# Kernel tuning notes

Hardware: AMD Instinct MI355X
Metric: run time of the kernel (lower is better)

Reference implementation:

```python
import jax, jax.numpy as jnp
import numpy as np


def _chain_marginals(u, p, g):
    """Gamma-smoothed forward-backward marginals on independent chains.
    u: [N, L, K] unaries, p: [N, L-1, K, K] pairwise (prev-state, next-state), g: scalar temperature.
    Returns marginals [N, L, K] (softmax of smoothed max-marginals).
    """
    u_t = jnp.swapaxes(u, 0, 1)   # [L, N, K]
    p_t = jnp.swapaxes(p, 0, 1)   # [L-1, N, K, K]

    def fstep(a, xs):
        ui, pi = xs  # ui: [N,K] at i, pi: [N,K,K] edge (i-1,i)
        a_new = ui + g * jax.nn.logsumexp((a[:, :, None] + pi) / g, axis=1)
        return a_new, a_new

    a0 = u_t[0]
    _, alpha_rest = jax.lax.scan(fstep, a0, (u_t[1:], p_t))
    alpha = jnp.concatenate([a0[None], alpha_rest], axis=0)  # [L,N,K]

    def bstep(b, xs):
        ui, pi = xs  # ui: unary at i+1, pi: edge (i, i+1)
        b_new = g * jax.nn.logsumexp(((ui + b)[:, None, :] + pi) / g, axis=2)
        return b_new, b_new

    bL = jnp.zeros_like(a0)
    _, beta_head = jax.lax.scan(bstep, bL, (u_t[1:], p_t), reverse=True)
    beta = jnp.concatenate([beta_head, bL[None]], axis=0)  # [L,N,K]

    m = jax.nn.softmax((alpha + beta) / g, axis=-1)
    return jnp.swapaxes(m, 0, 1)  # [N,L,K]


def setup_inputs() -> dict:
    key = jax.random.key(0)
    ks = jax.random.split(key, 4)
    B, K, H, W = 4, 21, 256, 256
    return {
        "unary_h": jax.random.normal(ks[0], (B, K, H, W), dtype=jnp.float32),
        "unary_v": jax.random.normal(ks[1], (B, K, H, W), dtype=jnp.float32),
        "pairwise_h": jax.random.normal(ks[2], (B, K, K, H, W - 1), dtype=jnp.float32),
        "pairwise_v": jax.random.normal(ks[3], (B, K, K, H - 1, W), dtype=jnp.float32),
        "gamma": jnp.ones((1,), dtype=jnp.float32),
    }


def reference(unary_h, unary_v, pairwise_h, pairwise_v, gamma):
    g = jnp.maximum(gamma[0], 0.01)  # module clamps learned gamma to >= 0.01
    B, K, H, W = unary_h.shape

    # Horizontal chains: one chain per (b, h) row, length W.
    uh = unary_h.transpose(0, 2, 3, 1).reshape(B * H, W, K)
    ph = pairwise_h.transpose(0, 3, 4, 1, 2).reshape(B * H, W - 1, K, K)
    mh = _chain_marginals(uh, ph, g).reshape(B, H, W, K).transpose(0, 3, 1, 2)

    # Vertical chains: one chain per (b, w) column, length H.
    uv = unary_v.transpose(0, 3, 2, 1).reshape(B * W, H, K)
    pv = pairwise_v.transpose(0, 4, 3, 1, 2).reshape(B * W, H - 1, K, K)
    mv = _chain_marginals(uv, pv, g).reshape(B, W, H, K).transpose(0, 3, 2, 1)

    avg = (mh + mv) * 0.5
    new_uh = unary_h - (mh - avg) / W
    new_uv = unary_v - (mv - avg) / H
    return new_uh, new_uv, mh, mv
```

## Files before the change

### kernel.cpp

```cpp
#include <hip/hip_runtime.h>


#define K 21
#define KP 22
#define TT 8
#define HP 256
#define NE 255
#define ROWF (K*KP)
#define TILEF (TT*ROWF)
#define EUF (TT*K)
#define NT 32
#define SZ (4*K*HP*HP)

__device__ __forceinline__ float rlane(float v, int l) {
  return __int_as_float(__builtin_amdgcn_readlane(__float_as_int(v), l));
}

__global__ __launch_bounds__(384)
void fp_scan_kernel(const float* __restrict__ uh, const float* __restrict__ uv,
                    const float* __restrict__ ph, const float* __restrict__ pv,
                    const float* __restrict__ gam, float* out) {
  __shared__ float smem[2*TILEF + 2*EUF];
  const float g = fmaxf(gam[0], 0.01f);
  const float invg = 1.0f / g;
  float* outMH = out + 2L*SZ;
  float* outMV = out + 3L*SZ;
  const int wg = blockIdx.x;
  const int tid = threadIdx.x;

  if (wg < 64) {
    const int b   = wg >> 4;
    const int wc0 = (wg & 15) << 4;
    const int kIdx = tid >> 4;
    const int c    = tid & 15;
    const int kk   = (kIdx < K) ? kIdx : (K-1);
    const bool pred = (kIdx < K);
    float* bc = smem;

    const long uBase = ((long)(b*K + kk)*HP)*HP + wc0 + c;
    const long kStep = (long)NE*HP;

    float pA[K], pB[K];

    {
      const long pfBase = (((long)(b*K)*K + kk)*NE)*HP + wc0 + c;
      float ea = __expf(uv[uBase] * invg);
      if (pred) outMV[uBase] = ea;
      #pragma unroll
      for (int k2 = 0; k2 < K; ++k2) pA[k2] = pv[pfBase + (long)k2*K*kStep];
      float uA = uv[uBase + 1L*HP], uB;

      auto fstep = [&](int i, const float* P, float uN, float ea_) -> float {
        bc[(i&1)*336 + kk*16 + c] = ea_;
        __syncthreads();
        const float* bb = bc + (i&1)*336 + c;
        float y0 = fmaxf(bb[0], 1e-33f);
        float s0=0.f, s1=0.f, s2=0.f;
        #pragma unroll
        for (int k2 = 0; k2 < K; k2 += 3) {
          s0 = fmaf(__expf(P[k2  ]*invg), bb[(k2  )*16], s0);
          s1 = fmaf(__expf(P[k2+1]*invg), bb[(k2+1)*16], s1);
          s2 = fmaf(__expf(P[k2+2]*invg), bb[(k2+2)*16], s2);
        }
        float r = (((s0+s1)+s2) / y0) * __expf(uN*invg);
        if (pred) outMV[uBase + (long)(i+1)*HP] = r;
        return r;
      };

      for (int i = 0; i < 254; i += 2) {
        #pragma unroll
        for (int k2=0;k2<K;++k2) pB[k2] = pv[pfBase + (long)k2*K*kStep + (long)(i+1)*HP];
        uB = uv[uBase + (long)(i+2)*HP];
        ea = fstep(i, pA, uA, ea);
        #pragma unroll
        for (int k2=0;k2<K;++k2) pA[k2] = pv[pfBase + (long)k2*K*kStep + (long)(i+2)*HP];
        uA = uv[uBase + (long)(i+3)*HP];
        ea = fstep(i+1, pB, uB, ea);
      }
      ea = fstep(254, pA, uA, ea);
    }
    __syncthreads();
    {
      const long pbBase = (((long)(b*K + kk)*K)*NE)*HP + wc0 + c;
      float eb = 1.0f;
      #pragma unroll
      for (int k2=0;k2<K;++k2) pA[k2] = pv[pbBase + (long)k2*kStep + 254L*HP];
      float uA  = uv[uBase + 255L*HP], uB;
      float eaA = outMV[uBase + 254L*HP], eaB;

      auto bstep = [&](int i, const float* P, float uN, float eaP, float eb_) -> float {
        float y = eb_ * __expf(uN*invg);
        bc[(i&1)*336 + kk*16 + c] = y;
        __syncthreads();
        const float* bb = bc + (i&1)*336 + c;
        float y0 = fmaxf(bb[0], 1e-33f);
        float s0=0.f, s1=0.f, s2=0.f;
        #pragma unroll
        for (int k2 = 0; k2 < K; k2 += 3) {
          s0 = fmaf(__expf(P[k2  ]*invg), bb[(k2  )*16], s0);
          s1 = fmaf(__expf(P[k2+1]*invg), bb[(k2+1)*16], s1);
          s2 = fmaf(__expf(P[k2+2]*invg), bb[(k2+2)*16], s2);
        }
        float r = ((s0+s1)+s2) / y0;
        if (pred) outMV[uBase + (long)i*HP] = eaP * r;
        return r;
      };

      for (int i = 254; i >= 2; i -= 2) {
        #pragma unroll
        for (int k2=0;k2<K;++k2) pB[k2] = pv[pbBase + (long)k2*kStep + (long)(i-1)*HP];
        uB  = uv[uBase + (long)i*HP];
        eaB = outMV[uBase + (long)(i-1)*HP];
        eb = bstep(i, pA, uA, eaA, eb);
        #pragma unroll
        for (int k2=0;k2<K;++k2) pA[k2] = pv[pbBase + (long)k2*kStep + (long)((i-2>0)?(i-2):0)*HP];
        uA  = uv[uBase + (long)(i-1)*HP];
        eaA = outMV[uBase + (long)((i-2>0)?(i-2):0)*HP];
        eb = bstep(i-1, pB, uB, eaB, eb);
      }
      eb = bstep(0, pA, uA, eaA, eb);
    }
  } else {
    const int id = wg - 64;
    const int b = id >> 8;
    const int h = id & 255;
    const int lane   = tid & 63;
    const int waveId = tid >> 6;
    const int stid   = tid - 64;
    const int cc  = (lane < K) ? lane : (K-1);
    const bool act = (lane < K) && (waveId == 0);
    float* EuBase = smem + 2*TILEF;

    auto stage = [&](int it, int phase) {
      float* Pb = smem  + (it & 1)*TILEF;
      float* Eb = EuBase + (it & 1)*EUF;
      const int w0 = it * TT;
      for (int idx = stid; idx < 3696; idx += 320) {
        if (idx < 3528) {
          int row = idx >> 3, t = idx & 7;
          int k = row / K, kp = row - k*K;
          int w = min(w0 + t, NE-1);
          float val = ph[(((long)(b*K + k)*K + kp)*HP + h)*(long)NE + w];
          float e = __expf(val * invg);
          int a  = phase ? k : kp;
          int b2 = phase ? kp : k;
          Pb[t*ROWF + a*KP + b2] = e;
        } else {
          int r = idx - 3528;
          int kk2 = r >> 3, t = r & 7;
          int pos = min(w0 + 1 + t, HP-1);
          float val = uh[((long)(b*K + kk2)*HP + h)*HP + pos];
          Eb[t*K + kk2] = __expf(val * invg);
        }
      }
    };

    const long chanBase = ((long)(b*K + cc)*HP + h)*HP;

    float ea = 0.f;
    if (waveId == 0) {
      ea = __expf(uh[chanBase] * invg);
      if (act) outMH[chanBase] = ea;
    }
    if (waveId > 0) stage(0, 0);
    __syncthreads();
    for (int it = 0; it < NT; ++it) {
      if (waveId > 0) {
        if (it + 1 < NT) stage(it + 1, 0);
      } else {
        float* Pb = smem  + (it & 1)*TILEF;
        float* Eb = EuBase + (it & 1)*EUF;
        const int w0 = it * TT;
        const int tt = min(TT, NE - w0);
        for (int t = 0; t < tt; ++t) {
          const float* row = Pb + t*ROWF + cc*KP;
          float s0=0.f, s1=0.f, s2=0.f;
          #pragma unroll
          for (int k2 = 0; k2 < K; k2 += 3) {
            s0 = fmaf(row[k2  ], rlane(ea, k2  ), s0);
            s1 = fmaf(row[k2+1], rlane(ea, k2+1), s1);
            s2 = fmaf(row[k2+2], rlane(ea, k2+2), s2);
          }
          float v  = ((s0+s1)+s2) * Eb[t*K + cc];
          float v0 = fmaxf(rlane(v, 0), 1e-33f);
          ea = v / v0;
          if (act) outMH[chanBase + (w0 + t + 1)] = ea;
        }
      }
      __syncthreads();
    }
    float eb = 1.0f;
    float eaPref = 0.f;
    if (waveId == 0) eaPref = outMH[chanBase + (NE-1)];
    if (waveId > 0) stage(NT-1, 1);
    __syncthreads();
    for (int it = NT-1; it >= 0; --it) {
      if (waveId > 0) {
        if (it > 0) stage(it - 1, 1);
      } else {
        float* Pb = smem  + (it & 1)*TILEF;
        float* Eb = EuBase + (it & 1)*EUF;
        const int w0 = it * TT;
        const int tt = min(TT, NE - w0);
        for (int t = tt - 1; t >= 0; --t) {
          float y = eb * Eb[t*K + cc];
          const float* row = Pb + t*ROWF + cc*KP;
          float s0=0.f, s1=0.f, s2=0.f;
          #pragma unroll
          for (int k2 = 0; k2 < K; k2 += 3) {
            s0 = fmaf(row[k2  ], rlane(y, k2  ), s0);
            s1 = fmaf(row[k2+1], rlane(y, k2+1), s1);
            s2 = fmaf(row[k2+2], rlane(y, k2+2), s2);
          }
          float s  = (s0+s1)+s2;
          float v0 = fmaxf(rlane(s, 0), 1e-33f);
          eb = s / v0;
          float prod = eaPref * eb;
          int pos = w0 + t;
          eaPref = outMH[chanBase + max(pos - 1, 0)];
          if (act) outMH[chanBase + pos] = prod;
        }
      }
      __syncthreads();
    }
  }
}

__global__ __launch_bounds__(256)
void fp_combine_kernel(const float* __restrict__ uh, const float* __restrict__ uv,
                       float* __restrict__ out) {
  const int lin = blockIdx.x * 256 + threadIdx.x;
  const int b   = lin >> 16;
  const int rem = lin & 65535;
  const long base = (long)b * K * 65536 + rem;
  const long KS = 65536;
  float mh[K], mv[K];
  float smh = 0.f, smv = 0.f;
  #pragma unroll
  for (int k = 0; k < K; ++k) {
    mh[k] = out[2L*SZ + base + k*KS];
    mv[k] = out[3L*SZ + base + k*KS];
    smh += mh[k]; smv += mv[k];
  }
  const float rh = 1.0f / smh, rv = 1.0f / smv;
  #pragma unroll
  for (int k = 0; k < K; ++k) {
    float a  = mh[k] * rh;
    float vv = mv[k] * rv;
    float d  = (a - vv) * (1.0f / 512.0f);
    out[        base + k*KS] = uh[base + k*KS] - d;
    out[1L*SZ + base + k*KS] = uv[base + k*KS] + d;
    out[2L*SZ + base + k*KS] = a;
    out[3L*SZ + base + k*KS] = vv;
  }
}

extern "C" void kernel_launch(void* const* d_in, const int* in_sizes, int n_in,
                              void* d_out, int out_size, void* d_ws, size_t ws_size,
                              hipStream_t stream) {
  const float* uh = (const float*)d_in[0];
  const float* uv = (const float*)d_in[1];
  const float* ph = (const float*)d_in[2];
  const float* pv = (const float*)d_in[3];
  const float* gm = (const float*)d_in[4];
  float* out = (float*)d_out;
  hipLaunchKernelGGL(fp_scan_kernel,    dim3(1088), dim3(384), 0, stream, uh, uv, ph, pv, gm, out);
  hipLaunchKernelGGL(fp_combine_kernel, dim3(1024), dim3(256), 0, stream, uh, uv, out);
}
```

Baseline: 1.922 ms.

## Double tile depth, batch staging loads, use 32-bit offsets and fast exp2/rcp

```diff
diff --git a/kernel.cpp b/kernel.cpp
--- a/kernel.cpp
+++ b/kernel.cpp
@@ -3,17 +3,26 @@
 
 #define K 21
 #define KP 22
-#define TT 8
+#define TT 16
 #define HP 256
 #define NE 255
 #define ROWF (K*KP)
 #define TILEF (TT*ROWF)
 #define EUF (TT*K)
-#define NT 32
+#define NT 16
+#define NP (K*K*TT)
 #define SZ (4*K*HP*HP)
+#define KS4 261120u
+#define KS4K 5483520u
 
 __device__ __forceinline__ float rlane(float v, int l) {
   return __int_as_float(__builtin_amdgcn_readlane(__float_as_int(v), l));
+}
+__device__ __forceinline__ float ldu(const float* p, unsigned off) {
+  return *(const float*)((const char*)p + off);
+}
+__device__ __forceinline__ void stu(float* p, unsigned off, float v) {
+  *(float*)((char*)p + off) = v;
 }
 
 __global__ __launch_bounds__(384)
@@ -21,8 +30,8 @@
                     const float* __restrict__ ph, const float* __restrict__ pv,
                     const float* __restrict__ gam, float* out) {
   __shared__ float smem[2*TILEF + 2*EUF];
-  const float g = fmaxf(gam[0], 0.01f);
-  const float invg = 1.0f / g;
+  const float g  = fmaxf(gam[0], 0.01f);
+  const float c2 = 1.44269504088896341f / g;
   float* outMH = out + 2L*SZ;
   float* outMV = out + 3L*SZ;
   const int wg = blockIdx.x;
@@ -37,18 +46,16 @@
     const bool pred = (kIdx < K);
     float* bc = smem;
 
-    const long uBase = ((long)(b*K + kk)*HP)*HP + wc0 + c;
-    const long kStep = (long)NE*HP;
-
+    const unsigned uB4 = ((unsigned)((b*K + kk)*HP)*HP + wc0 + c) * 4u;
     float pA[K], pB[K];
 
     {
-      const long pfBase = (((long)(b*K)*K + kk)*NE)*HP + wc0 + c;
-      float ea = __expf(uv[uBase] * invg);
-      if (pred) outMV[uBase] = ea;
+      const unsigned pf4 = ((unsigned)(b*K*K + kk)*(NE*HP) + wc0 + c) * 4u;
+      float ea = exp2f(ldu(uv, uB4) * c2);
+      if (pred) stu(outMV, uB4, ea);
       #pragma unroll
-      for (int k2 = 0; k2 < K; ++k2) pA[k2] = pv[pfBase + (long)k2*K*kStep];
-      float uA = uv[uBase + 1L*HP], uB;
+      for (int k2 = 0; k2 < K; ++k2) pA[k2] = ldu(pv, pf4 + (unsigned)k2*KS4K);
+      float uA = ldu(uv, uB4 + 1024u), uB;
 
       auto fstep = [&](int i, const float* P, float uN, float ea_) -> float {
         bc[(i&1)*336 + kk*16 + c] = ea_;
@@ -58,38 +65,40 @@
         float s0=0.f, s1=0.f, s2=0.f;
         #pragma unroll
         for (int k2 = 0; k2 < K; k2 += 3) {
-          s0 = fmaf(__expf(P[k2  ]*invg), bb[(k2  )*16], s0);
-          s1 = fmaf(__expf(P[k2+1]*invg), bb[(k2+1)*16], s1);
-          s2 = fmaf(__expf(P[k2+2]*invg), bb[(k2+2)*16], s2);
-        }
-        float r = (((s0+s1)+s2) / y0) * __expf(uN*invg);
-        if (pred) outMV[uBase + (long)(i+1)*HP] = r;
+          s0 = fmaf(exp2f(P[k2  ]*c2), bb[(k2  )*16], s0);
+          s1 = fmaf(exp2f(P[k2+1]*c2), bb[(k2+1)*16], s1);
+          s2 = fmaf(exp2f(P[k2+2]*c2), bb[(k2+2)*16], s2);
+        }
+        float r = (((s0+s1)+s2) * __builtin_amdgcn_rcpf(y0)) * exp2f(uN*c2);
+        if (pred) stu(outMV, uB4 + (unsigned)(i+1)*1024u, r);
         return r;
       };
 
       for (int i = 0; i < 254; i += 2) {
-        #pragma unroll
-        for (int k2=0;k2<K;++k2) pB[k2] = pv[pfBase + (long)k2*K*kStep + (long)(i+1)*HP];
-        uB = uv[uBase + (long)(i+2)*HP];
+        const unsigned o1 = pf4 + (unsigned)(i+1)*1024u;
+        #pragma unroll
+        for (int k2=0;k2<K;++k2) pB[k2] = ldu(pv, o1 + (unsigned)k2*KS4K);
+        uB = ldu(uv, uB4 + (unsigned)(i+2)*1024u);
         ea = fstep(i, pA, uA, ea);
-        #pragma unroll
-        for (int k2=0;k2<K;++k2) pA[k2] = pv[pfBase + (long)k2*K*kStep + (long)(i+2)*HP];
-        uA = uv[uBase + (long)(i+3)*HP];
+        const unsigned o2 = pf4 + (unsigned)(i+2)*1024u;
+        #pragma unroll
+        for (int k2=0;k2<K;++k2) pA[k2] = ldu(pv, o2 + (unsigned)k2*KS4K);
+        uA = ldu(uv, uB4 + (unsigned)(i+3)*1024u);
         ea = fstep(i+1, pB, uB, ea);
       }
       ea = fstep(254, pA, uA, ea);
     }
     __syncthreads();
     {
-      const long pbBase = (((long)(b*K + kk)*K)*NE)*HP + wc0 + c;
+      const unsigned pb4 = ((unsigned)((b*K + kk)*K)*(NE*HP) + wc0 + c) * 4u;
       float eb = 1.0f;
       #pragma unroll
-      for (int k2=0;k2<K;++k2) pA[k2] = pv[pbBase + (long)k2*kStep + 254L*HP];
-      float uA  = uv[uBase + 255L*HP], uB;
-      float eaA = outMV[uBase + 254L*HP], eaB;
+      for (int k2=0;k2<K;++k2) pA[k2] = ldu(pv, pb4 + (unsigned)k2*KS4 + 254u*1024u);
+      float uA  = ldu(uv, uB4 + 255u*1024u), uB;
+      float eaA = ldu(outMV, uB4 + 254u*1024u), eaB;
 
       auto bstep = [&](int i, const float* P, float uN, float eaP, float eb_) -> float {
-        float y = eb_ * __expf(uN*invg);
+        float y = eb_ * exp2f(uN*c2);
         bc[(i&1)*336 + kk*16 + c] = y;
         __syncthreads();
         const float* bb = bc + (i&1)*336 + c;
@@ -97,25 +106,28 @@
         float s0=0.f, s1=0.f, s2=0.f;
         #pragma unroll
         for (int k2 = 0; k2 < K; k2 += 3) {
-          s0 = fmaf(__expf(P[k2  ]*invg), bb[(k2  )*16], s0);
-          s1 = fmaf(__expf(P[k2+1]*invg), bb[(k2+1)*16], s1);
-          s2 = fmaf(__expf(P[k2+2]*invg), bb[(k2+2)*16], s2);
-        }
-        float r = ((s0+s1)+s2) / y0;
-        if (pred) outMV[uBase + (long)i*HP] = eaP * r;
+          s0 = fmaf(exp2f(P[k2  ]*c2), bb[(k2  )*16], s0);
+          s1 = fmaf(exp2f(P[k2+1]*c2), bb[(k2+1)*16], s1);
+          s2 = fmaf(exp2f(P[k2+2]*c2), bb[(k2+2)*16], s2);
+        }
+        float r = ((s0+s1)+s2) * __builtin_amdgcn_rcpf(y0);
+        if (pred) stu(outMV, uB4 + (unsigned)i*1024u, eaP * r);
         return r;
       };
 
       for (int i = 254; i >= 2; i -= 2) {
-        #pragma unroll
-        for (int k2=0;k2<K;++k2) pB[k2] = pv[pbBase + (long)k2*kStep + (long)(i-1)*HP];
-        uB  = uv[uBase + (long)i*HP];
-        eaB = outMV[uBase + (long)(i-1)*HP];
+        const unsigned o1 = pb4 + (unsigned)(i-1)*1024u;
+        #pragma unroll
+        for (int k2=0;k2<K;++k2) pB[k2] = ldu(pv, o1 + (unsigned)k2*KS4);
+        uB  = ldu(uv, uB4 + (unsigned)i*1024u);
+        eaB = ldu(outMV, uB4 + (unsigned)(i-1)*1024u);
         eb = bstep(i, pA, uA, eaA, eb);
-        #pragma unroll
-        for (int k2=0;k2<K;++k2) pA[k2] = pv[pbBase + (long)k2*kStep + (long)((i-2>0)?(i-2):0)*HP];
-        uA  = uv[uBase + (long)(i-1)*HP];
-        eaA = outMV[uBase + (long)((i-2>0)?(i-2):0)*HP];
+        const int im2 = (i-2>0)?(i-2):0;
+        const unsigned o2 = pb4 + (unsigned)im2*1024u;
+        #pragma unroll
+        for (int k2=0;k2<K;++k2) pA[k2] = ldu(pv, o2 + (unsigned)k2*KS4);
+        uA  = ldu(uv, uB4 + (unsigned)(i-1)*1024u);
+        eaA = ldu(outMV, uB4 + (unsigned)im2*1024u);
         eb = bstep(i-1, pB, uB, eaB, eb);
       }
       eb = bstep(0, pA, uA, eaA, eb);
@@ -131,36 +143,55 @@
     const bool act = (lane < K) && (waveId == 0);
     float* EuBase = smem + 2*TILEF;
 
+    const unsigned phB = (unsigned)(b*(K*K))*KS4 + (unsigned)(h*NE)*4u;
+    const unsigned uhB = (unsigned)(b*K*HP + h)*(HP*4u);
+
     auto stage = [&](int it, int phase) {
       float* Pb = smem  + (it & 1)*TILEF;
       float* Eb = EuBase + (it & 1)*EUF;
       const int w0 = it * TT;
-      for (int idx = stid; idx < 3696; idx += 320) {
-        if (idx < 3528) {
-          int row = idx >> 3, t = idx & 7;
+      float vP[23], vE0, vE1;
+      #pragma unroll
+      for (int j = 0; j < 23; ++j) {
+        int idx = stid + j*320;
+        idx = (idx < NP) ? idx : (NP-1);
+        int row = idx >> 4, t = idx & 15;
+        int w = w0 + t; w = (w < NE) ? w : (NE-1);
+        vP[j] = ldu(ph, phB + (unsigned)row*KS4 + (unsigned)w*4u);
+      }
+      {
+        int r0 = (stid < EUF) ? stid : (EUF-1);
+        int p0 = w0 + 1 + (r0 & 15); p0 = (p0 < HP) ? p0 : (HP-1);
+        vE0 = ldu(uh, uhB + (unsigned)(r0 >> 4)*(HP*HP*4u) + (unsigned)p0*4u);
+        int r1 = (stid + 320 < EUF) ? (stid + 320) : (EUF-1);
+        int p1 = w0 + 1 + (r1 & 15); p1 = (p1 < HP) ? p1 : (HP-1);
+        vE1 = ldu(uh, uhB + (unsigned)(r1 >> 4)*(HP*HP*4u) + (unsigned)p1*4u);
+      }
+      #pragma unroll
+      for (int j = 0; j < 23; ++j) {
+        int idx = stid + j*320;
+        if (idx < NP) {
+          float e = exp2f(vP[j] * c2);
+          int row = idx >> 4, t = idx & 15;
           int k = row / K, kp = row - k*K;
-          int w = min(w0 + t, NE-1);
-          float val = ph[(((long)(b*K + k)*K + kp)*HP + h)*(long)NE + w];
-          float e = __expf(val * invg);
           int a  = phase ? k : kp;
           int b2 = phase ? kp : k;
           Pb[t*ROWF + a*KP + b2] = e;
-        } else {
-          int r = idx - 3528;
-          int kk2 = r >> 3, t = r & 7;
-          int pos = min(w0 + 1 + t, HP-1);
-          float val = uh[((long)(b*K + kk2)*HP + h)*HP + pos];
-          Eb[t*K + kk2] = __expf(val * invg);
-        }
+        }
+      }
+      if (stid < EUF) Eb[(stid & 15)*K + (stid >> 4)] = exp2f(vE0 * c2);
+      {
+        int r1 = stid + 320;
+        if (r1 < EUF) Eb[(r1 & 15)*K + (r1 >> 4)] = exp2f(vE1 * c2);
       }
     };
 
-    const long chanBase = ((long)(b*K + cc)*HP + h)*HP;
+    const unsigned chB = (unsigned)((b*K + cc)*HP + h)*(HP*4u);
 
     float ea = 0.f;
     if (waveId == 0) {
-      ea = __expf(uh[chanBase] * invg);
-      if (act) outMH[chanBase] = ea;
+      ea = exp2f(ldu(uh, chB) * c2);
+      if (act) stu(outMH, chB, ea);
     }
     if (waveId > 0) stage(0, 0);
     __syncthreads();
@@ -183,15 +214,15 @@
           }
           float v  = ((s0+s1)+s2) * Eb[t*K + cc];
           float v0 = fmaxf(rlane(v, 0), 1e-33f);
-          ea = v / v0;
-          if (act) outMH[chanBase + (w0 + t + 1)] = ea;
+          ea = v * __builtin_amdgcn_rcpf(v0);
+          if (act) stu(outMH, chB + (unsigned)(w0 + t + 1)*4u, ea);
         }
       }
       __syncthreads();
     }
     float eb = 1.0f;
     float eaPref = 0.f;
-    if (waveId == 0) eaPref = outMH[chanBase + (NE-1)];
+    if (waveId == 0) eaPref = ldu(outMH, chB + (unsigned)(NE-1)*4u);
     if (waveId > 0) stage(NT-1, 1);
     __syncthreads();
     for (int it = NT-1; it >= 0; --it) {
@@ -214,11 +245,11 @@
           }
           float s  = (s0+s1)+s2;
           float v0 = fmaxf(rlane(s, 0), 1e-33f);
-          eb = s / v0;
+          eb = s * __builtin_amdgcn_rcpf(v0);
           float prod = eaPref * eb;
           int pos = w0 + t;
-          eaPref = outMH[chanBase + max(pos - 1, 0)];
-          if (act) outMH[chanBase + pos] = prod;
+          eaPref = ldu(outMH, chB + (unsigned)max(pos - 1, 0)*4u);
+          if (act) stu(outMH, chB + (unsigned)pos*4u, prod);
         }
       }
       __syncthreads();
```

After: 1.745 ms. -9.2%, faster.
